# Performance work log

Hardware: AMD Instinct MI355X
Metric: run time of the kernel (lower is better)

The kernel has to match this reference:

```python
import jax, jax.numpy as jnp
import numpy as np
import math

N, L, S, H, E, D = 2, 2048, 2048, 16, 64, 64

def setup_inputs() -> dict:
    key = jax.random.key(0)
    kq, kk, kv = jax.random.split(key, 3)
    return {
        "queries": jax.random.normal(kq, (N, L, H, E), dtype=jnp.float32),
        "keys": jax.random.normal(kk, (N, S, H, E), dtype=jnp.float32),
        "values": jax.random.normal(kv, (N, S, H, D), dtype=jnp.float32),
        "attn_mask": jnp.zeros((L, S), dtype=jnp.float32),  # additive mask
    }

def reference(queries, keys, values, attn_mask):
    e = queries.shape[-1]
    softmax_temp = 1.0 / math.sqrt(e)  # self.softmax_temp is None -> 1/sqrt(E)
    # (N,L,H,E) x (N,S,H,E) -> (N,H,L,S)
    qk = jnp.einsum('nlhe,nshe->nhls', queries, keys)
    qk = qk + attn_mask  # additive mask broadcast over (N,H)
    att = jax.nn.softmax(softmax_temp * qk, axis=-1)
    # dropout rate 0.0 (eval) -> identity
    v = jnp.einsum('nhls,nshd->nlhd', att, values)
    return v
```

## Files before the change

kernel.cpp:

```cpp
#include <hip/hip_runtime.h>
#include <hip/hip_bf16.h>


typedef short bf16x8 __attribute__((ext_vector_type(8)));
typedef short short4v __attribute__((ext_vector_type(4)));
typedef unsigned uint2v __attribute__((ext_vector_type(2)));
typedef unsigned uint4v __attribute__((ext_vector_type(4)));
typedef float f32x4 __attribute__((ext_vector_type(4)));

constexpr int Nb = 2, Lq = 2048, Sk = 2048, Hh = 16, Ee = 64, Dd = 64;
constexpr int BM = 256;
constexpr int BN = 64;
constexpr int NT = Sk / BN;
constexpr int KVB = 4096;
constexpr int MSKB = 2048;
constexpr float SCALE_LOG2E = 0.125f * 1.4426950408889634f;

__device__ __forceinline__ short f2bf(float f) {
  union { float f; unsigned u; } v; v.f = f;
  unsigned r = (v.u + 0x7fffu + ((v.u >> 16) & 1u)) >> 16;
  return (short)r;
}

__device__ __forceinline__ unsigned pack_bf16x2(float a, float b) {
  union { __hip_bfloat162 h; unsigned u; } v;
  float2 f; f.x = a; f.y = b;
  v.h = __float22bfloat162_rn(f);
  return v.u;
}

__device__ __forceinline__ float bf_lo(unsigned u) { return __uint_as_float(u << 16); }
__device__ __forceinline__ float bf_hi(unsigned u) { return __uint_as_float(u & 0xffff0000u); }

__device__ __forceinline__ void async_copy16(const void* g, void* l) {
  __builtin_amdgcn_global_load_lds(
      (const __attribute__((address_space(1))) unsigned int*)g,
      (__attribute__((address_space(3))) unsigned int*)l, 16, 0, 0);
}

__global__ __launch_bounds__(256) void prep_all(const float* __restrict__ K,
                                                const float* __restrict__ V,
                                                const float* __restrict__ M,
                                                short* __restrict__ KVf,
                                                short* __restrict__ Mg) {
  if (blockIdx.x < KVB) {
    int gid = blockIdx.x * 256 + threadIdx.x;
    int off8 = gid & 1023;
    int t  = (gid >> 10) & 31;
    int nh = gid >> 15;
    int n = nh >> 4, h = nh & 15;
    short* dst = KVf + ((size_t)(nh * NT + t)) * 8192 + off8 * 8;
    if (off8 < 512) {
      int ch = off8 >> 6;
      int l  = off8 & 63;
      int sb = ch >> 1, kc = ch & 1, c = l & 15, quad = l >> 4;
      const float* p = K + (((size_t)n * Sk + (t * 64 + sb * 16 + c)) * Hh + h) * Ee
                         + kc * 32 + quad * 8;
      float4 x = *(const float4*)(p);
      float4 y = *(const float4*)(p + 4);
      bf16x8 o;
      o[0] = f2bf(x.x); o[1] = f2bf(x.y); o[2] = f2bf(x.z); o[3] = f2bf(x.w);
      o[4] = f2bf(y.x); o[5] = f2bf(y.y); o[6] = f2bf(y.z); o[7] = f2bf(y.w);
      *(bf16x8*)dst = o;
    } else {
      int pos = off8 - 512;
      int chunk = pos >> 6;
      int l = pos & 63;
      int db = chunk >> 1, sbp = chunk & 1, cc = l & 15, quad = l >> 4;
      const float* pbase = V + (((size_t)n * Sk + (t * 64 + sbp * 32 + quad * 4)) * Hh + h) * Dd
                             + db * 16 + cc;
      bf16x8 o;
#pragma unroll
      for (int k = 0; k < 8; ++k) {
        int s_off = (k >> 2) * 16 + (k & 3);
        o[k] = f2bf(pbase[(size_t)s_off * Hh * Dd]);
      }
      *(bf16x8*)dst = o;
    }
  } else {
    int u = (blockIdx.x - KVB) * 256 + threadIdx.x;
    int sub  = u & 7;
    int lane = (u >> 3) & 63;
    int t    = (u >> 9) & 31;
    int qw   = u >> 14;
    int cb = sub >> 1, sbp = sub & 1;
    int c = lane & 15, quad = lane >> 4;
    int row = (qw >> 2) * 256 + (qw & 3) * 64 + cb * 16 + c;
    short o[8];
#pragma unroll
    for (int k = 0; k < 2; ++k) {
      int sb = sbp * 2 + k;
      float4 mv = *(const float4*)(M + (size_t)row * Sk + t * 64 + sb * 16 + quad * 4);
      o[k * 4 + 0] = f2bf(mv.x * SCALE_LOG2E);
      o[k * 4 + 1] = f2bf(mv.y * SCALE_LOG2E);
      o[k * 4 + 2] = f2bf(mv.z * SCALE_LOG2E);
      o[k * 4 + 3] = f2bf(mv.w * SCALE_LOG2E);
    }
    *(bf16x8*)(Mg + (size_t)u * 8) = *(const bf16x8*)o;
  }
}

template <int NS>
__global__ __launch_bounds__(256, 2) void attn_fwd(
    const float* __restrict__ Q, const short* __restrict__ KVf,
    const short* __restrict__ Mg, float* __restrict__ P0,
    float* __restrict__ P1, float* __restrict__ rsW)
{
  __shared__ short KV[3][8192];

  const int tid  = threadIdx.x;
  const int lane = tid & 63;
  const int w    = tid >> 6;
  const int quad = lane >> 4;
  const int c    = lane & 15;

  const int id   = blockIdx.x;
  const int slot = id >> 3;
  const int nh   = (id & 7) * 4 + (slot & 3);
  const int qt   = (slot >> 2) & 7;
  const int sp   = (NS == 2) ? (slot >> 5) : 0;
  const int n    = nh >> 4;
  const int h    = nh & 15;

  const int row0 = qt * BM + w * 64;
  const int t0 = sp * (NT / NS), tc = NT / NS;

  bf16x8 qfrag[4][2];
#pragma unroll
  for (int cb = 0; cb < 4; ++cb) {
    const float* qp = Q + (((size_t)n * Lq + (row0 + cb * 16 + c)) * Hh + h) * Ee;
#pragma unroll
    for (int kc = 0; kc < 2; ++kc) {
      const float* p = qp + kc * 32 + quad * 8;
      float4 x = *(const float4*)(p);
      float4 y = *(const float4*)(p + 4);
      bf16x8 f;
      f[0] = f2bf(x.x * SCALE_LOG2E); f[1] = f2bf(x.y * SCALE_LOG2E);
      f[2] = f2bf(x.z * SCALE_LOG2E); f[3] = f2bf(x.w * SCALE_LOG2E);
      f[4] = f2bf(y.x * SCALE_LOG2E); f[5] = f2bf(y.y * SCALE_LOG2E);
      f[6] = f2bf(y.z * SCALE_LOG2E); f[7] = f2bf(y.w * SCALE_LOG2E);
      qfrag[cb][kc] = f;
    }
  }

  f32x4 o[4][4];
#pragma unroll
  for (int cb = 0; cb < 4; ++cb)
#pragma unroll
    for (int db = 0; db < 4; ++db) { o[cb][db][0] = 0.f; o[cb][db][1] = 0.f; o[cb][db][2] = 0.f; o[cb][db][3] = 0.f; }
  float rs[4] = {0.f, 0.f, 0.f, 0.f};

  const short* kvt = KVf + (size_t)nh * NT * 8192;
  const short* mbase = Mg + (size_t)(qt * 4 + w) * 131072 + lane * 64;

  uint4v mcur[8];
#pragma unroll
  for (int i = 0; i < 8; ++i) mcur[i] = *(const uint4v*)(mbase + (size_t)t0 * 4096 + i * 8);
#pragma unroll
  for (int i = 0; i < 4; ++i) {
    int seg = w * 4 + i;
    async_copy16(kvt + ((size_t)t0 * 8192) + seg * 512 + lane * 8, &KV[0][seg * 512 + lane * 8]);
  }
#pragma unroll
  for (int i = 0; i < 4; ++i) {
    int seg = w * 4 + i;
    async_copy16(kvt + ((size_t)(t0 + 1) * 8192) + seg * 512 + lane * 8, &KV[1][seg * 512 + lane * 8]);
  }
  asm volatile("s_waitcnt vmcnt(4)" ::: "memory");
  __builtin_amdgcn_s_barrier();

  int bR = 0;
  for (int tt = 0; tt < tc; ++tt) {
    const int t = t0 + tt;
    const short* kb = &KV[bR][0];

    f32x4 sacc[4][4];
#pragma unroll
    for (int cb = 0; cb < 4; ++cb)
#pragma unroll
      for (int sbp = 0; sbp < 2; ++sbp) {
        uint4v m = mcur[cb * 2 + sbp];
        sacc[cb][sbp * 2 + 0][0] = bf_lo(m.x); sacc[cb][sbp * 2 + 0][1] = bf_hi(m.x);
        sacc[cb][sbp * 2 + 0][2] = bf_lo(m.y); sacc[cb][sbp * 2 + 0][3] = bf_hi(m.y);
        sacc[cb][sbp * 2 + 1][0] = bf_lo(m.z); sacc[cb][sbp * 2 + 1][1] = bf_hi(m.z);
        sacc[cb][sbp * 2 + 1][2] = bf_lo(m.w); sacc[cb][sbp * 2 + 1][3] = bf_hi(m.w);
      }

    if (tt + 1 < tc) {
      const short* gm = mbase + (size_t)(t + 1) * 4096;
#pragma unroll
      for (int i = 0; i < 8; ++i) mcur[i] = *(const uint4v*)(gm + i * 8);
    }
    if (tt + 2 < tc) {
      int bW = bR + 2; if (bW >= 3) bW -= 3;
      const short* gk = kvt + (size_t)(t + 2) * 8192;
      short* lw = &KV[bW][0];
#pragma unroll
      for (int i = 0; i < 4; ++i) {
        int seg = w * 4 + i;
        async_copy16(gk + seg * 512 + lane * 8, &lw[seg * 512 + lane * 8]);
      }
    }

    short4v pv[4][4];
#pragma unroll
    for (int sb = 0; sb < 4; ++sb) {
      bf16x8 kf0 = *(const bf16x8*)&kb[(sb * 2 + 0) * 512 + lane * 8];
      bf16x8 kf1 = *(const bf16x8*)&kb[(sb * 2 + 1) * 512 + lane * 8];
#pragma unroll
      for (int cb = 0; cb < 4; ++cb) {
        sacc[cb][sb] = __builtin_amdgcn_mfma_f32_16x16x32_bf16(kf0, qfrag[cb][0], sacc[cb][sb], 0, 0, 0);
        sacc[cb][sb] = __builtin_amdgcn_mfma_f32_16x16x32_bf16(kf1, qfrag[cb][1], sacc[cb][sb], 0, 0, 0);
      }
      if (sb > 0) {
        const int sl = sb - 1;
#pragma unroll
        for (int cb = 0; cb < 4; ++cb) {
          float p0 = __builtin_amdgcn_exp2f(sacc[cb][sl][0]);
          float p1 = __builtin_amdgcn_exp2f(sacc[cb][sl][1]);
          float p2 = __builtin_amdgcn_exp2f(sacc[cb][sl][2]);
          float p3 = __builtin_amdgcn_exp2f(sacc[cb][sl][3]);
          rs[cb] += (p0 + p1) + (p2 + p3);
          union { uint2v u; short4v s; } uu;
          uu.u.x = pack_bf16x2(p0, p1);
          uu.u.y = pack_bf16x2(p2, p3);
          pv[cb][sl] = uu.s;
        }
      }
    }
#pragma unroll
    for (int cb = 0; cb < 4; ++cb) {
      float p0 = __builtin_amdgcn_exp2f(sacc[cb][3][0]);
      float p1 = __builtin_amdgcn_exp2f(sacc[cb][3][1]);
      float p2 = __builtin_amdgcn_exp2f(sacc[cb][3][2]);
      float p3 = __builtin_amdgcn_exp2f(sacc[cb][3][3]);
      rs[cb] += (p0 + p1) + (p2 + p3);
      union { uint2v u; short4v s; } uu;
      uu.u.x = pack_bf16x2(p0, p1);
      uu.u.y = pack_bf16x2(p2, p3);
      pv[cb][3] = uu.s;
    }

#pragma unroll
    for (int db = 0; db < 4; ++db) {
#pragma unroll
      for (int sbp = 0; sbp < 2; ++sbp) {
        bf16x8 vv = *(const bf16x8*)&kb[4096 + (db * 2 + sbp) * 512 + lane * 8];
        short4v v0, v1;
        v0[0] = vv[0]; v0[1] = vv[1]; v0[2] = vv[2]; v0[3] = vv[3];
        v1[0] = vv[4]; v1[1] = vv[5]; v1[2] = vv[6]; v1[3] = vv[7];
#pragma unroll
        for (int cb = 0; cb < 4; ++cb) {
          o[cb][db] = __builtin_amdgcn_mfma_f32_16x16x16bf16_1k(v0, pv[cb][sbp * 2 + 0], o[cb][db], 0, 0, 0);
          o[cb][db] = __builtin_amdgcn_mfma_f32_16x16x16bf16_1k(v1, pv[cb][sbp * 2 + 1], o[cb][db], 0, 0, 0);
        }
      }
    }

    asm volatile("s_waitcnt vmcnt(4)" ::: "memory");
    __builtin_amdgcn_s_barrier();
    bR += 1; if (bR == 3) bR = 0;
  }

  float* P = (sp == 0) ? P0 : P1;
#pragma unroll
  for (int cb = 0; cb < 4; ++cb) {
    float v = rs[cb];
    v += __shfl_xor(v, 16, 64);
    v += __shfl_xor(v, 32, 64);
    const int qrow = row0 + cb * 16 + c;
    if (quad == 0) rsW[(size_t)sp * 65536 + nh * 2048 + qrow] = v;
    float* op = P + (((size_t)n * Lq + qrow) * Hh + h) * Dd + quad * 4;
#pragma unroll
    for (int db = 0; db < 4; ++db) {
      float4 ov;
      ov.x = o[cb][db][0]; ov.y = o[cb][db][1];
      ov.z = o[cb][db][2]; ov.w = o[cb][db][3];
      *(float4*)(op + db * 16) = ov;
    }
  }
}

template <int NS>
__global__ __launch_bounds__(256) void combine(float* __restrict__ Out,
                                               const float* __restrict__ P1,
                                               const float* __restrict__ rsW) {
  int gid = blockIdx.x * 256 + threadIdx.x;
  size_t i4 = (size_t)gid * 4;
  int hh = (int)((i4 >> 6) & 15);
  int l  = (int)((i4 >> 10) & 2047);
  int nn = (int)(i4 >> 21);
  int nh = nn * 16 + hh;
  float rs = rsW[nh * 2048 + l];
  float4 v = *(const float4*)(Out + i4);
  if (NS == 2) {
    rs += rsW[65536 + (size_t)nh * 2048 + l];
    float4 b = *(const float4*)(P1 + i4);
    v.x += b.x; v.y += b.y; v.z += b.z; v.w += b.w;
  }
  float inv = 1.0f / rs;
  v.x *= inv; v.y *= inv; v.z *= inv; v.w *= inv;
  *(float4*)(Out + i4) = v;
}

extern "C" void kernel_launch(void* const* d_in, const int* in_sizes, int n_in,
                              void* d_out, int out_size, void* d_ws, size_t ws_size,
                              hipStream_t stream) {
  const float* Q   = (const float*)d_in[0];
  const float* K   = (const float*)d_in[1];
  const float* V   = (const float*)d_in[2];
  const float* Msk = (const float*)d_in[3];
  float* Out = (float*)d_out;

  short* KVf = (short*)d_ws;
  short* Mg  = KVf + (size_t)8388608;
  float* rsW = (float*)(Mg + (size_t)4194304);
  float* P1  = rsW + 131072;

  const size_t need2 = 16777216u + 8388608u + 524288u + 16777216u;
  const bool split = ws_size >= need2;

  prep_all<<<dim3(KVB + MSKB), dim3(256), 0, stream>>>(K, V, Msk, KVf, Mg);

  if (split) {
    attn_fwd<2><<<dim3(512), dim3(256), 0, stream>>>(Q, KVf, Mg, Out, P1, rsW);
    combine<2><<<dim3(4096), dim3(256), 0, stream>>>(Out, P1, rsW);
  } else {
    attn_fwd<1><<<dim3(256), dim3(256), 0, stream>>>(Q, KVf, Mg, Out, P1, rsW);
    combine<1><<<dim3(4096), dim3(256), 0, stream>>>(Out, P1, rsW);
  }
}
```

Measured before the change: 167.6 us.

## Halve query tile and drop KV split plus combine kernel

Measured after the change: 151.1 us, median of 3. 1.11x faster.

```diff
diff --git a/kernel.cpp b/kernel.cpp
--- a/kernel.cpp
+++ b/kernel.cpp
@@ -9,7 +9,7 @@
 typedef float f32x4 __attribute__((ext_vector_type(4)));
 
 constexpr int Nb = 2, Lq = 2048, Sk = 2048, Hh = 16, Ee = 64, Dd = 64;
-constexpr int BM = 256;
+constexpr int BM = 128;
 constexpr int BN = 64;
 constexpr int NT = Sk / BN;
 constexpr int KVB = 4096;
@@ -79,13 +79,13 @@
     }
   } else {
     int u = (blockIdx.x - KVB) * 256 + threadIdx.x;
-    int sub  = u & 7;
-    int lane = (u >> 3) & 63;
-    int t    = (u >> 9) & 31;
-    int qw   = u >> 14;
+    int sub  = u & 3;
+    int lane = (u >> 2) & 63;
+    int t    = (u >> 8) & 31;
+    int qw   = u >> 13;
     int cb = sub >> 1, sbp = sub & 1;
     int c = lane & 15, quad = lane >> 4;
-    int row = (qw >> 2) * 256 + (qw & 3) * 64 + cb * 16 + c;
+    int row = (qw >> 2) * 128 + (qw & 3) * 32 + cb * 16 + c;
     short o[8];
 #pragma unroll
     for (int k = 0; k < 2; ++k) {
@@ -100,11 +100,9 @@
   }
 }
 
-template <int NS>
 __global__ __launch_bounds__(256, 2) void attn_fwd(
     const float* __restrict__ Q, const short* __restrict__ KVf,
-    const short* __restrict__ Mg, float* __restrict__ P0,
-    float* __restrict__ P1, float* __restrict__ rsW)
+    const short* __restrict__ Mg, float* __restrict__ Out)
 {
   __shared__ short KV[3][8192];
 
@@ -117,17 +115,16 @@
   const int id   = blockIdx.x;
   const int slot = id >> 3;
   const int nh   = (id & 7) * 4 + (slot & 3);
-  const int qt   = (slot >> 2) & 7;
-  const int sp   = (NS == 2) ? (slot >> 5) : 0;
+  const int qt   = (slot >> 2) & 15;
   const int n    = nh >> 4;
   const int h    = nh & 15;
 
-  const int row0 = qt * BM + w * 64;
-  const int t0 = sp * (NT / NS), tc = NT / NS;
-
-  bf16x8 qfrag[4][2];
-#pragma unroll
-  for (int cb = 0; cb < 4; ++cb) {
+  const int row0 = qt * BM + w * 32;
+  constexpr int tc = NT;
+
+  bf16x8 qfrag[2][2];
+#pragma unroll
+  for (int cb = 0; cb < 2; ++cb) {
     const float* qp = Q + (((size_t)n * Lq + (row0 + cb * 16 + c)) * Hh + h) * Ee;
 #pragma unroll
     for (int kc = 0; kc < 2; ++kc) {
@@ -143,40 +140,39 @@
     }
   }
 
-  f32x4 o[4][4];
-#pragma unroll
-  for (int cb = 0; cb < 4; ++cb)
+  f32x4 o[2][4];
+#pragma unroll
+  for (int cb = 0; cb < 2; ++cb)
 #pragma unroll
     for (int db = 0; db < 4; ++db) { o[cb][db][0] = 0.f; o[cb][db][1] = 0.f; o[cb][db][2] = 0.f; o[cb][db][3] = 0.f; }
-  float rs[4] = {0.f, 0.f, 0.f, 0.f};
+  float rs[2] = {0.f, 0.f};
 
   const short* kvt = KVf + (size_t)nh * NT * 8192;
-  const short* mbase = Mg + (size_t)(qt * 4 + w) * 131072 + lane * 64;
-
-  uint4v mcur[8];
-#pragma unroll
-  for (int i = 0; i < 8; ++i) mcur[i] = *(const uint4v*)(mbase + (size_t)t0 * 4096 + i * 8);
+  const short* mbase = Mg + (size_t)(qt * 4 + w) * 65536 + lane * 32;
+
+  uint4v mcur[4];
+#pragma unroll
+  for (int i = 0; i < 4; ++i) mcur[i] = *(const uint4v*)(mbase + i * 8);
 #pragma unroll
   for (int i = 0; i < 4; ++i) {
     int seg = w * 4 + i;
-    async_copy16(kvt + ((size_t)t0 * 8192) + seg * 512 + lane * 8, &KV[0][seg * 512 + lane * 8]);
+    async_copy16(kvt + seg * 512 + lane * 8, &KV[0][seg * 512 + lane * 8]);
   }
 #pragma unroll
   for (int i = 0; i < 4; ++i) {
     int seg = w * 4 + i;
-    async_copy16(kvt + ((size_t)(t0 + 1) * 8192) + seg * 512 + lane * 8, &KV[1][seg * 512 + lane * 8]);
+    async_copy16(kvt + 8192 + seg * 512 + lane * 8, &KV[1][seg * 512 + lane * 8]);
   }
   asm volatile("s_waitcnt vmcnt(4)" ::: "memory");
   __builtin_amdgcn_s_barrier();
 
   int bR = 0;
   for (int tt = 0; tt < tc; ++tt) {
-    const int t = t0 + tt;
     const short* kb = &KV[bR][0];
 
-    f32x4 sacc[4][4];
-#pragma unroll
-    for (int cb = 0; cb < 4; ++cb)
+    f32x4 sacc[2][4];
+#pragma unroll
+    for (int cb = 0; cb < 2; ++cb)
 #pragma unroll
       for (int sbp = 0; sbp < 2; ++sbp) {
         uint4v m = mcur[cb * 2 + sbp];
@@ -187,13 +183,13 @@
       }
 
     if (tt + 1 < tc) {
-      const short* gm = mbase + (size_t)(t + 1) * 4096;
-#pragma unroll
-      for (int i = 0; i < 8; ++i) mcur[i] = *(const uint4v*)(gm + i * 8);
+      const short* gm = mbase + (size_t)(tt + 1) * 2048;
+#pragma unroll
+      for (int i = 0; i < 4; ++i) mcur[i] = *(const uint4v*)(gm + i * 8);
     }
     if (tt + 2 < tc) {
       int bW = bR + 2; if (bW >= 3) bW -= 3;
-      const short* gk = kvt + (size_t)(t + 2) * 8192;
+      const short* gk = kvt + (size_t)(tt + 2) * 8192;
       short* lw = &KV[bW][0];
 #pragma unroll
       for (int i = 0; i < 4; ++i) {
@@ -202,20 +198,20 @@
       }
     }
 
-    short4v pv[4][4];
+    short4v pv[2][4];
 #pragma unroll
     for (int sb = 0; sb < 4; ++sb) {
       bf16x8 kf0 = *(const bf16x8*)&kb[(sb * 2 + 0) * 512 + lane * 8];
       bf16x8 kf1 = *(const bf16x8*)&kb[(sb * 2 + 1) * 512 + lane * 8];
 #pragma unroll
-      for (int cb = 0; cb < 4; ++cb) {
+      for (int cb = 0; cb < 2; ++cb) {
         sacc[cb][sb] = __builtin_amdgcn_mfma_f32_16x16x32_bf16(kf0, qfrag[cb][0], sacc[cb][sb], 0, 0, 0);
         sacc[cb][sb] = __builtin_amdgcn_mfma_f32_16x16x32_bf16(kf1, qfrag[cb][1], sacc[cb][sb], 0, 0, 0);
       }
       if (sb > 0) {
         const int sl = sb - 1;
 #pragma unroll
-        for (int cb = 0; cb < 4; ++cb) {
+        for (int cb = 0; cb < 2; ++cb) {
           float p0 = __builtin_amdgcn_exp2f(sacc[cb][sl][0]);
           float p1 = __builtin_amdgcn_exp2f(sacc[cb][sl][1]);
           float p2 = __builtin_amdgcn_exp2f(sacc[cb][sl][2]);
@@ -229,7 +225,7 @@
       }
     }
 #pragma unroll
-    for (int cb = 0; cb < 4; ++cb) {
+    for (int cb = 0; cb < 2; ++cb) {
       float p0 = __builtin_amdgcn_exp2f(sacc[cb][3][0]);
       float p1 = __builtin_amdgcn_exp2f(sacc[cb][3][1]);
       float p2 = __builtin_amdgcn_exp2f(sacc[cb][3][2]);
@@ -250,7 +246,7 @@
         v0[0] = vv[0]; v0[1] = vv[1]; v0[2] = vv[2]; v0[3] = vv[3];
         v1[0] = vv[4]; v1[1] = vv[5]; v1[2] = vv[6]; v1[3] = vv[7];
 #pragma unroll
-        for (int cb = 0; cb < 4; ++cb) {
+        for (int cb = 0; cb < 2; ++cb) {
           o[cb][db] = __builtin_amdgcn_mfma_f32_16x16x16bf16_1k(v0, pv[cb][sbp * 2 + 0], o[cb][db], 0, 0, 0);
           o[cb][db] = __builtin_amdgcn_mfma_f32_16x16x16bf16_1k(v1, pv[cb][sbp * 2 + 1], o[cb][db], 0, 0, 0);
         }
@@ -262,45 +258,22 @@
     bR += 1; if (bR == 3) bR = 0;
   }
 
-  float* P = (sp == 0) ? P0 : P1;
-#pragma unroll
-  for (int cb = 0; cb < 4; ++cb) {
+#pragma unroll
+  for (int cb = 0; cb < 2; ++cb) {
     float v = rs[cb];
     v += __shfl_xor(v, 16, 64);
     v += __shfl_xor(v, 32, 64);
+    const float inv = 1.0f / v;
     const int qrow = row0 + cb * 16 + c;
-    if (quad == 0) rsW[(size_t)sp * 65536 + nh * 2048 + qrow] = v;
-    float* op = P + (((size_t)n * Lq + qrow) * Hh + h) * Dd + quad * 4;
+    float* op = Out + (((size_t)n * Lq + qrow) * Hh + h) * Dd + quad * 4;
 #pragma unroll
     for (int db = 0; db < 4; ++db) {
       float4 ov;
-      ov.x = o[cb][db][0]; ov.y = o[cb][db][1];
-      ov.z = o[cb][db][2]; ov.w = o[cb][db][3];
+      ov.x = o[cb][db][0] * inv; ov.y = o[cb][db][1] * inv;
+      ov.z = o[cb][db][2] * inv; ov.w = o[cb][db][3] * inv;
       *(float4*)(op + db * 16) = ov;
     }
   }
-}
-
-template <int NS>
-__global__ __launch_bounds__(256) void combine(float* __restrict__ Out,
-                                               const float* __restrict__ P1,
-                                               const float* __restrict__ rsW) {
-  int gid = blockIdx.x * 256 + threadIdx.x;
-  size_t i4 = (size_t)gid * 4;
-  int hh = (int)((i4 >> 6) & 15);
-  int l  = (int)((i4 >> 10) & 2047);
-  int nn = (int)(i4 >> 21);
-  int nh = nn * 16 + hh;
-  float rs = rsW[nh * 2048 + l];
-  float4 v = *(const float4*)(Out + i4);
-  if (NS == 2) {
-    rs += rsW[65536 + (size_t)nh * 2048 + l];
-    float4 b = *(const float4*)(P1 + i4);
-    v.x += b.x; v.y += b.y; v.z += b.z; v.w += b.w;
-  }
-  float inv = 1.0f / rs;
-  v.x *= inv; v.y *= inv; v.z *= inv; v.w *= inv;
-  *(float4*)(Out + i4) = v;
 }
 
 extern "C" void kernel_launch(void* const* d_in, const int* in_sizes, int n_in,
@@ -314,19 +287,7 @@
 
   short* KVf = (short*)d_ws;
   short* Mg  = KVf + (size_t)8388608;
-  float* rsW = (float*)(Mg + (size_t)4194304);
-  float* P1  = rsW + 131072;
-
-  const size_t need2 = 16777216u + 8388608u + 524288u + 16777216u;
-  const bool split = ws_size >= need2;
 
   prep_all<<<dim3(KVB + MSKB), dim3(256), 0, stream>>>(K, V, Msk, KVf, Mg);
-
-  if (split) {
-    attn_fwd<2><<<dim3(512), dim3(256), 0, stream>>>(Q, KVf, Mg, Out, P1, rsW);
-    combine<2><<<dim3(4096), dim3(256), 0, stream>>>(Out, P1, rsW);
-  } else {
-    attn_fwd<1><<<dim3(256), dim3(256), 0, stream>>>(Q, KVf, Mg, Out, P1, rsW);
-    combine<1><<<dim3(4096), dim3(256), 0, stream>>>(Out, P1, rsW);
-  }
-}
+  attn_fwd<<<dim3(512), dim3(256), 0, stream>>>(Q, KVf, Mg, Out);
+}
```
